# Kernel optimization log

Measured on AMD Instinct MI355X. Metric: run time of the kernel, lower is better.

## Reference

```python
import jax, jax.numpy as jnp
import numpy as np

IMAGE_H, IMAGE_W = 256, 704
Z, Y, X = 128, 8, 128
BOUNDS = (-50.0, 50.0, -5.0, 5.0, -50.0, 50.0)
CENTROID = (0.0, 1.0, 0.0)
EPS_MEAN = 1e-6
EPS_DEPTH = 1e-4


def _compose_rt(R, t):
    M = jnp.zeros(R.shape[:-2] + (4, 4), R.dtype)
    M = M.at[..., :3, :3].set(R)
    M = M.at[..., :3, 3].set(t)
    M = M.at[..., 3, 3].set(1.0)
    return M


def _safe_inverse(M):
    R = M[..., :3, :3]
    t = M[..., :3, 3]
    Rt = jnp.swapaxes(R, -1, -2)
    return _compose_rt(Rt, -jnp.einsum('...ij,...j->...i', Rt, t))


def _apply_4x4(M, xyz):
    # M: (...,4,4), xyz: (...,N,3) -> (...,N,3)
    return jnp.einsum('...ij,...nj->...ni', M[..., :3, :3], xyz) + M[..., None, :3, 3]


def _xyz_camA():
    # Mem2Ref of gridcloud3d: x_ref = x_mem*vox + MIN + vox/2 (bounds shifted by centroid)
    xmin = BOUNDS[0] + CENTROID[0]; xmax = BOUNDS[1] + CENTROID[0]
    ymin = BOUNDS[2] + CENTROID[1]; ymax = BOUNDS[3] + CENTROID[1]
    zmin = BOUNDS[4] + CENTROID[2]; zmax = BOUNDS[5] + CENTROID[2]
    vx = (xmax - xmin) / X; vy = (ymax - ymin) / Y; vz = (zmax - zmin) / Z
    zz, yy, xx = jnp.meshgrid(jnp.arange(Z, dtype=jnp.float32),
                              jnp.arange(Y, dtype=jnp.float32),
                              jnp.arange(X, dtype=jnp.float32), indexing='ij')
    x = xx * vx + xmin + vx / 2.0
    y = yy * vy + ymin + vy / 2.0
    z = zz * vz + zmin + vz / 2.0
    return jnp.stack([x, y, z], -1).reshape(Z * Y * X, 3)  # mem order (Z,Y,X)


def _bilinear_sample(img, px, py):
    # img: (C,H,W); px,py: (N,) pixel coords; zeros padding (grid_sample align_corners=False)
    C, H, W = img.shape
    x0 = jnp.floor(px); y0 = jnp.floor(py)
    dx = px - x0; dy = py - y0
    x0i = x0.astype(jnp.int32); y0i = y0.astype(jnp.int32)
    flat = img.reshape(C, H * W)

    def gather(yi, xi, w):
        inb = (xi >= 0) & (xi < W) & (yi >= 0) & (yi < H)
        idx = jnp.clip(yi, 0, H - 1) * W + jnp.clip(xi, 0, W - 1)
        return flat[:, idx] * (w * inb.astype(img.dtype))

    return (gather(y0i, x0i, (1 - dx) * (1 - dy))
            + gather(y0i, x0i + 1, dx * (1 - dy))
            + gather(y0i + 1, x0i, (1 - dx) * dy)
            + gather(y0i + 1, x0i + 1, dx * dy))  # (C,N)


def _forward(cam_feat, camera2ego, cam_intrinsic, conv_w):
    B, S, C, Hf, Wf = cam_feat.shape
    # velo_T_cams = merge_rt(camera2ego R, t); cam0_T_camXs = inv(velo_T_cams[:,0]) @ velo_T_cams
    velo_T_cams = _compose_rt(camera2ego[..., :3, :3], camera2ego[..., :3, 3])
    cam0_T_velo = _safe_inverse(velo_T_cams[:, 0])
    cam0_T_camXs = jnp.einsum('bij,bsjk->bsik', cam0_T_velo, velo_T_cams)
    camXs_T_cam0 = _safe_inverse(cam0_T_camXs)
    # scale_intrinsics with sy = Hf/H*0.284, sx = Wf/W*0.44
    sy = Hf / float(IMAGE_H) * 0.284
    sx = Wf / float(IMAGE_W) * 0.44
    fx = cam_intrinsic[..., 0, 0] * sx
    fy = cam_intrinsic[..., 1, 1] * sy
    cx = cam_intrinsic[..., 0, 2] * sx
    cy = cam_intrinsic[..., 1, 2] * sy
    K = jnp.zeros((B, S, 4, 4), cam_feat.dtype)
    K = K.at[..., 0, 0].set(fx).at[..., 1, 1].set(fy)
    K = K.at[..., 0, 2].set(cx).at[..., 1, 2].set(cy)
    K = K.at[..., 2, 2].set(1.0).at[..., 3, 3].set(1.0)
    pixB_T_cam0 = jnp.einsum('bsij,bsjk->bsik', K, camXs_T_cam0)

    xyz = _xyz_camA()  # (N,3), N = Z*Y*X
    xyz_camB = _apply_4x4(camXs_T_cam0, xyz[None, None])  # (B,S,N,3)
    z_cam = xyz_camB[..., 2]
    xyz_pix = _apply_4x4(pixB_T_cam0, xyz[None, None])
    depth = jnp.maximum(xyz_pix[..., 2], EPS_DEPTH)
    x_pix = xyz_pix[..., 0] / depth
    y_pix = xyz_pix[..., 1] / depth
    valid = ((x_pix > -0.5) & (x_pix < Wf - 0.5)
             & (y_pix > -0.5) & (y_pix < Hf - 0.5)
             & (z_cam > 0.0)).astype(cam_feat.dtype)
    # normalize_grid2d (clamp [-2,2]) then grid_sample align_corners=False unnormalize
    gx = jnp.clip(2.0 * x_pix / (Wf - 1) - 1.0, -2.0, 2.0)
    gy = jnp.clip(2.0 * y_pix / (Hf - 1) - 1.0, -2.0, 2.0)
    px = ((gx + 1.0) * Wf - 1.0) / 2.0
    py = ((gy + 1.0) * Hf - 1.0) / 2.0

    feats = cam_feat.reshape(B * S, C, Hf, Wf)
    vals = jax.vmap(_bilinear_sample)(feats, px.reshape(B * S, -1), py.reshape(B * S, -1))
    vals = vals.reshape(B, S, C, -1) * valid[:, :, None, :]  # (B,S,C,N)
    mask = (jnp.abs(vals) > 0).astype(vals.dtype)
    feat_mem = jnp.sum(vals * mask, axis=1) / (EPS_MEAN + jnp.sum(mask, axis=1))  # (B,C,N)
    feat_mem = feat_mem.reshape(B, C, Z, Y, X)

    # BEV compress: permute(0,1,3,2,4) -> (B, C*Y, Z, X), conv3x3 (no bias), InstanceNorm2d, GELU
    feat_bev = jnp.transpose(feat_mem, (0, 1, 3, 2, 4)).reshape(B, C * Y, Z, X)
    out = jax.lax.conv_general_dilated(feat_bev, conv_w, (1, 1), ((1, 1), (1, 1)),
                                       dimension_numbers=('NCHW', 'OIHW', 'NCHW'))
    mu = jnp.mean(out, axis=(2, 3), keepdims=True)
    var = jnp.var(out, axis=(2, 3), keepdims=True)
    out = (out - mu) / jnp.sqrt(var + 1e-5)
    return jax.nn.gelu(out, approximate=False)


def setup_inputs() -> dict:
    key = jax.random.key(0)
    k1, k2, k3 = jax.random.split(key, 3)
    B, S, C, Hf, Wf = 1, 6, 128, 32, 88
    cam_feat = jax.random.normal(k1, (B, S, C, Hf, Wf), jnp.float32)
    # rigid camera2ego: yaw rotations about the y axis + small translations
    yaws = jnp.arange(S, dtype=jnp.float32) * (2.0 * jnp.pi / S)
    c, s = jnp.cos(yaws), jnp.sin(yaws)
    zr, on = jnp.zeros_like(c), jnp.ones_like(c)
    R = jnp.stack([jnp.stack([c, zr, s], -1),
                   jnp.stack([zr, on, zr], -1),
                   jnp.stack([-s, zr, c], -1)], -2)  # (S,3,3)
    t = jax.random.normal(k2, (S, 3), jnp.float32) * 0.5
    cam2ego = jnp.zeros((B, S, 4, 4), jnp.float32)
    cam2ego = cam2ego.at[0, :, :3, :3].set(R).at[0, :, :3, 3].set(t).at[0, :, 3, 3].set(1.0)
    K = jnp.zeros((B, S, 4, 4), jnp.float32)
    K = K.at[..., 0, 0].set(600.0).at[..., 1, 1].set(600.0)
    K = K.at[..., 0, 2].set(352.0).at[..., 1, 2].set(128.0)
    K = K.at[..., 2, 2].set(1.0).at[..., 3, 3].set(1.0)
    conv_w = jax.random.normal(k3, (128, 128 * Y, 3, 3), jnp.float32) / np.sqrt(128 * Y * 9.0).astype(np.float32)
    return {"cam_feat": cam_feat, "camera2ego": cam2ego, "cam_intrinsic": K, "conv_w": conv_w}


def reference(cam_feat, camera2ego, cam_intrinsic, conv_w):
    return _forward(cam_feat, camera2ego, cam_intrinsic, conv_w)
```

## Files before the change

kernel.cpp:

```cpp
#include <hip/hip_runtime.h>
#include <hip/hip_bf16.h>
#include <math.h>

#define HF 32
#define WF 88
#define NCAM 6
#define CC 128
#define ZD 128
#define YD 8
#define XD 128

using f32x4  = __attribute__((ext_vector_type(4))) float;
using bf16x8 = __attribute__((ext_vector_type(8))) short;

#define OFF_P    0ull
#define OFF_W    512ull
#define OFF_CAMT (OFF_W + 2359296ull)
#define OFF_F    (OFF_CAMT + 8650752ull)
#define OFF_CONV (OFF_F + 34611200ull)

__global__ __launch_bounds__(64) void k0_mats(const float* __restrict__ cam2ego,
                                              const float* __restrict__ intr,
                                              float* __restrict__ P) {
  int s = threadIdx.x;
  if (s >= NCAM) return;
  const float* M0 = cam2ego;
  const float* Ms = cam2ego + s * 16;
  float Rb[9], tb[3];
  for (int i = 0; i < 3; i++)
    for (int j = 0; j < 3; j++) {
      float v = 0.f;
      for (int k = 0; k < 3; k++) v += Ms[k * 4 + i] * M0[k * 4 + j];
      Rb[i * 3 + j] = v;
    }
  for (int i = 0; i < 3; i++) {
    float v = 0.f;
    for (int k = 0; k < 3; k++) v += Ms[k * 4 + i] * (M0[k * 4 + 3] - Ms[k * 4 + 3]);
    tb[i] = v;
  }
  const float* Ks = intr + s * 16;
  const float sx = (float)WF / 704.0f * 0.44f;
  const float sy = (float)HF / 256.0f * 0.284f;
  const float fx = Ks[0] * sx, fy = Ks[5] * sy;
  const float cx = Ks[2] * sx, cy = Ks[6] * sy;
  float* p = P + s * 12;
  for (int j = 0; j < 3; j++) p[j]     = fx * Rb[j]     + cx * Rb[6 + j];
  p[3]  = fx * tb[0] + cx * tb[2];
  for (int j = 0; j < 3; j++) p[4 + j] = fy * Rb[3 + j] + cy * Rb[6 + j];
  p[7]  = fy * tb[1] + cy * tb[2];
  for (int j = 0; j < 3; j++) p[8 + j] = Rb[6 + j];
  p[11] = tb[2];
}

__global__ __launch_bounds__(128) void k1_transpose(const float* __restrict__ feat,
                                                    __hip_bfloat16* __restrict__ camT) {
  const int b = blockIdx.x;
  const int wq = b & 3;
  const int sh = b >> 2;
  const int c = threadIdx.x;
  const float* src = feat + ((size_t)(sh / HF) * CC + c) * (HF * WF) + (sh % HF) * WF + wq * 22;
  __hip_bfloat16* dst = camT + ((size_t)sh * WF + wq * 22) * CC + c;
  for (int w = 0; w < 22; w++) dst[w * CC] = __float2bfloat16(src[w]);
}

__global__ __launch_bounds__(256) void k1b_packw(const float* __restrict__ w,
                                                 __hip_bfloat16* __restrict__ wp) {
  const int t = blockIdx.x * 256 + threadIdx.x;
  float v[9];
  #pragma unroll
  for (int d = 0; d < 9; d++) v[d] = w[(size_t)t * 9 + d];
  #pragma unroll
  for (int d = 0; d < 9; d++) wp[(size_t)d * 131072 + t] = __float2bfloat16(v[d]);
}

struct Rec { int off[4]; float w[4]; };

__global__ __launch_bounds__(256) void k2_sample(const __hip_bfloat16* __restrict__ camT,
                                                 const float* __restrict__ P,
                                                 __hip_bfloat16* __restrict__ F) {
  const int bz = blockIdx.x / 130;
  const int bx = blockIdx.x % 130;
  const int t = threadIdx.x;
  const int zi = bz - 1, xi = bx - 1;
  const int c = (t & 63) << 1;
  const int yq = t >> 6;
  __hip_bfloat16* Fb = F + (size_t)blockIdx.x * 1024;
  if (zi < 0 || zi >= ZD || xi < 0 || xi >= XD) {
    *reinterpret_cast<unsigned*>(Fb + c * 8 + yq * 2) = 0u;
    *reinterpret_cast<unsigned*>(Fb + (c + 1) * 8 + yq * 2) = 0u;
    return;
  }
  __shared__ Rec recs[48];
  if (t < 48) {
    const int y = t / 6, s = t - y * 6;
    const float* pp = P + s * 12;
    const float vx = 100.0f / 128.0f;
    const float xw = xi * vx - 50.0f + vx * 0.5f;
    const float zw = zi * vx - 50.0f + vx * 0.5f;
    const float yw = y * 1.25f - 4.0f + 0.625f;
    const float zc = pp[8] * xw + pp[9] * yw + pp[10] * zw + pp[11];
    const float xp = pp[0] * xw + pp[1] * yw + pp[2] * zw + pp[3];
    const float yp = pp[4] * xw + pp[5] * yw + pp[6] * zw + pp[7];
    const float dep = fmaxf(zc, 1e-4f);
    const float pxf = xp / dep, pyf = yp / dep;
    const bool valid = (pxf > -0.5f && pxf < (float)WF - 0.5f &&
                        pyf > -0.5f && pyf < (float)HF - 0.5f && zc > 0.0f);
    const float px = pxf * ((float)WF / (float)(WF - 1)) - 0.5f;
    const float py = pyf * ((float)HF / (float)(HF - 1)) - 0.5f;
    const float fx0 = floorf(px), fy0 = floorf(py);
    const float ddx = px - fx0, ddy = py - fy0;
    const int x0i = (int)fx0, y0i = (int)fy0;
    const float vf = valid ? 1.0f : 0.0f;
    float ww[4];
    ww[0] = (1.0f - ddx) * (1.0f - ddy) * vf;
    ww[1] = ddx * (1.0f - ddy) * vf;
    ww[2] = (1.0f - ddx) * ddy * vf;
    ww[3] = ddx * ddy * vf;
    const int cxs[4] = {x0i, x0i + 1, x0i, x0i + 1};
    const int cys[4] = {y0i, y0i, y0i + 1, y0i + 1};
    Rec r;
    #pragma unroll
    for (int k = 0; k < 4; k++) {
      const bool inb = ((unsigned)cxs[k] < WF) && ((unsigned)cys[k] < HF);
      const int xc = min(max(cxs[k], 0), WF - 1);
      const int yc = min(max(cys[k], 0), HF - 1);
      r.w[k] = inb ? ww[k] : 0.0f;
      r.off[k] = (s * (HF * WF) + yc * WF + xc) * CC;
    }
    recs[t] = r;
  }
  __syncthreads();

  float num[2][2] = {{0.f, 0.f}, {0.f, 0.f}};
  int cnt[2] = {0, 0};
  #pragma unroll
  for (int yi = 0; yi < 2; yi++) {
    const int y = yq * 2 + yi;
    for (int s = 0; s < NCAM; s++) {
      const Rec r = recs[y * 6 + s];
      if (r.w[0] == 0.f && r.w[1] == 0.f && r.w[2] == 0.f && r.w[3] == 0.f) continue;
      float v0 = 0.f, v1 = 0.f;
      #pragma unroll
      for (int k = 0; k < 4; k++) {
        const ushort2 uv = *reinterpret_cast<const ushort2*>(&camT[r.off[k] + c]);
        v0 += r.w[k] * __bfloat162float(*reinterpret_cast<const __hip_bfloat16*>(&uv.x));
        v1 += r.w[k] * __bfloat162float(*reinterpret_cast<const __hip_bfloat16*>(&uv.y));
      }
      num[yi][0] += v0;
      num[yi][1] += v1;
      cnt[yi]++;
    }
  }
  #pragma unroll
  for (int j = 0; j < 2; j++) {
    __hip_bfloat16 o[2];
    const float inv0 = 1.0f / (1e-6f + (float)cnt[0]);
    const float inv1 = 1.0f / (1e-6f + (float)cnt[1]);
    o[0] = __float2bfloat16(num[0][j] * inv0);
    o[1] = __float2bfloat16(num[1][j] * inv1);
    *reinterpret_cast<unsigned*>(Fb + (c + j) * 8 + yq * 2) =
        *reinterpret_cast<const unsigned*>(o);
  }
}

__device__ __forceinline__ void load_lds16(const void* g, void* l) {
  __builtin_amdgcn_global_load_lds(
      (const __attribute__((address_space(1))) unsigned int*)g,
      (__attribute__((address_space(3))) unsigned int*)l, 16, 0, 0);
}

#define K3_NT 36

__global__ __launch_bounds__(512) void k3_gemm(const __hip_bfloat16* __restrict__ F,
                                               const __hip_bfloat16* __restrict__ Wp,
                                               float* __restrict__ out0,
                                               float* __restrict__ out1) {
  const int orig = (blockIdx.x & 7) * 32 + (blockIdx.x >> 3);
  const int z = orig & 127;
  const int h = orig >> 7;
  const int ciH = h << 9;
  const int tid = threadIdx.x;
  const int w = tid >> 6;
  const int l = tid & 63;
  const int wm = w >> 2;
  const int wn = w & 3;
  __shared__ __hip_bfloat16 lds[65536];

  f32x4 acc[4][2];
  #pragma unroll
  for (int m = 0; m < 4; m++)
    #pragma unroll
    for (int n = 0; n < 2; n++)
      acc[m][n] = (f32x4){0.f, 0.f, 0.f, 0.f};

  auto stage_sub = [&](int sub) {
    const int base = ((sub >> 1) & 1) * 32768 + (sub & 1) * 16384;
    const int d = sub >> 3;
    const int dz = d / 3, dx = d - dz * 3;
    const int ci0 = ciH + ((sub & 7) << 6);
    const int zbase = (z + dz) * 130 + dx;
    #pragma unroll
    for (int i = 0; i < 2; i++) {
      const int n = w * 128 + i * 64 + l;
      const int row = n >> 3;
      const int q = (n & 7) ^ (row & 7);
      const __hip_bfloat16* src = F + ((size_t)(zbase + row) << 10) + ci0 + (q << 3);
      load_lds16(src, &lds[base + (w * 128 + i * 64) * 8]);
    }
    #pragma unroll
    for (int i = 0; i < 2; i++) {
      const int n = w * 128 + i * 64 + l;
      const int co = n >> 3;
      const int q = (n & 7) ^ (co & 7);
      const __hip_bfloat16* src = Wp + ((size_t)d << 17) + ((size_t)co << 10) + ci0 + (q << 3);
      load_lds16(src, &lds[base + 8192 + (w * 128 + i * 64) * 8]);
    }
  };
  auto stage = [&](int T) { stage_sub(2 * T); stage_sub(2 * T + 1); };

  auto compute_sub = [&](int base) {
    const int r16 = l & 15;
    const int hi = l >> 4;
    #pragma unroll
    for (int kk = 0; kk < 2; kk++) {
      const int c = kk * 4 + hi;
      bf16x8 a[4], b[2];
      #pragma unroll
      for (int m = 0; m < 4; m++) {
        const int r = wm * 64 + m * 16 + r16;
        const int slot = c ^ (r & 7);
        a[m] = *reinterpret_cast<const bf16x8*>(&lds[base + r * 64 + slot * 8]);
      }
      #pragma unroll
      for (int n = 0; n < 2; n++) {
        const int co = wn * 32 + n * 16 + r16;
        const int slot = c ^ (co & 7);
        b[n] = *reinterpret_cast<const bf16x8*>(&lds[base + 8192 + co * 64 + slot * 8]);
      }
      __builtin_amdgcn_s_setprio(1);
      #pragma unroll
      for (int m = 0; m < 4; m++)
        #pragma unroll
        for (int n = 0; n < 2; n++)
          acc[m][n] = __builtin_amdgcn_mfma_f32_16x16x32_bf16(a[m], b[n], acc[m][n], 0, 0, 0);
      __builtin_amdgcn_s_setprio(0);
    }
  };
  auto compute = [&](int T) {
    const int b0 = (T & 1) * 32768;
    compute_sub(b0);
    compute_sub(b0 + 16384);
  };

  stage(0); stage(1);
  asm volatile("s_waitcnt vmcnt(8)" ::: "memory");
  __builtin_amdgcn_s_barrier();

  for (int t = 0; t < K3_NT; ++t) {
    compute(t);
    __builtin_amdgcn_s_barrier();
    if (t + 2 < K3_NT) {
      stage(t + 2);
      asm volatile("s_waitcnt vmcnt(8)" ::: "memory");
    } else {
      asm volatile("s_waitcnt vmcnt(0)" ::: "memory");
    }
    __builtin_amdgcn_s_barrier();
  }

  float* outP = h ? out1 : out0;
  const int r16 = l & 15;
  const int hi = l >> 4;
  #pragma unroll
  for (int m = 0; m < 4; m++) {
    const int xr = wm * 64 + m * 16 + hi * 4;
    #pragma unroll
    for (int n = 0; n < 2; n++) {
      const int co = wn * 32 + n * 16 + r16;
      *reinterpret_cast<f32x4*>(&outP[((size_t)co << 14) + (z << 7) + xr]) = acc[m][n];
    }
  }
}

__device__ __forceinline__ float gelu_exact(float x) {
  return 0.5f * x * (1.0f + erff(x * 0.70710678118654752440f));
}

__global__ __launch_bounds__(256) void k4_ln(const float* __restrict__ c0,
                                             const float* __restrict__ c1,
                                             float* __restrict__ outp) {
  const int co = blockIdx.x;
  const float4* p0 = reinterpret_cast<const float4*>(c0 + ((size_t)co << 14));
  const float4* p1 = reinterpret_cast<const float4*>(c1 + ((size_t)co << 14));
  float4 v[16];
  float s = 0.f, s2 = 0.f;
  #pragma unroll
  for (int i = 0; i < 16; i++) {
    float4 a = p0[threadIdx.x + (i << 8)];
    float4 b = p1[threadIdx.x + (i << 8)];
    float4 t;
    t.x = a.x + b.x; t.y = a.y + b.y; t.z = a.z + b.z; t.w = a.w + b.w;
    v[i] = t;
    s  += t.x + t.y + t.z + t.w;
    s2 += t.x * t.x + t.y * t.y + t.z * t.z + t.w * t.w;
  }
  #pragma unroll
  for (int off = 32; off > 0; off >>= 1) {
    s  += __shfl_down(s, off);
    s2 += __shfl_down(s2, off);
  }
  __shared__ float red[8];
  __shared__ float mb[2];
  const int wv = threadIdx.x >> 6, ln = threadIdx.x & 63;
  if (ln == 0) { red[wv] = s; red[wv + 4] = s2; }
  __syncthreads();
  if (threadIdx.x == 0) {
    float S  = red[0] + red[1] + red[2] + red[3];
    float S2 = red[4] + red[5] + red[6] + red[7];
    float mu = S * (1.0f / 16384.0f);
    float var = S2 * (1.0f / 16384.0f) - mu * mu;
    mb[0] = mu;
    mb[1] = 1.0f / sqrtf(var + 1e-5f);
  }
  __syncthreads();
  const float mu = mb[0], inv = mb[1];
  float4* op = reinterpret_cast<float4*>(outp + ((size_t)co << 14));
  #pragma unroll
  for (int i = 0; i < 16; i++) {
    float4 t = v[i];
    float4 r;
    r.x = gelu_exact((t.x - mu) * inv);
    r.y = gelu_exact((t.y - mu) * inv);
    r.z = gelu_exact((t.z - mu) * inv);
    r.w = gelu_exact((t.w - mu) * inv);
    op[threadIdx.x + (i << 8)] = r;
  }
}

extern "C" void kernel_launch(void* const* d_in, const int* in_sizes, int n_in,
                              void* d_out, int out_size, void* d_ws, size_t ws_size,
                              hipStream_t stream) {
  const float* cam_feat = (const float*)d_in[0];
  const float* cam2ego  = (const float*)d_in[1];
  const float* intr     = (const float*)d_in[2];
  const float* conv_w   = (const float*)d_in[3];
  float* out = (float*)d_out;
  char* ws = (char*)d_ws;

  float*          P     = (float*)(ws + OFF_P);
  __hip_bfloat16* Wp    = (__hip_bfloat16*)(ws + OFF_W);
  __hip_bfloat16* camT  = (__hip_bfloat16*)(ws + OFF_CAMT);
  __hip_bfloat16* F     = (__hip_bfloat16*)(ws + OFF_F);
  float*          conv0 = (float*)(ws + OFF_CONV);
  float*          conv1 = (float*)(ws + OFF_CAMT);

  hipLaunchKernelGGL(k0_mats, dim3(1), dim3(64), 0, stream, cam2ego, intr, P);
  hipLaunchKernelGGL(k1_transpose, dim3(NCAM * HF * 4), dim3(128), 0, stream, cam_feat, camT);
  hipLaunchKernelGGL(k1b_packw, dim3(512), dim3(256), 0, stream, conv_w, Wp);
  hipLaunchKernelGGL(k2_sample, dim3(130 * 130), dim3(256), 0, stream, camT, P, F);
  hipLaunchKernelGGL(k3_gemm, dim3(256), dim3(512), 0, stream, F, Wp, conv0, conv1);
  hipLaunchKernelGGL(k4_ln, dim3(128), dim3(256), 0, stream, conv0, conv1, out);
}
```

Measured before the change: 115.6 us.

## Skip empty voxel columns in sampling and conv GEMM via validity bitmask

The sampling kernel now computes per-(z,x) validity with a ballot, exits early when no camera sees the column, and records validity in a global bitmask. The conv GEMM reads the bitmask for its 3-row z neighbourhood, then skips F loads, LDS reads and MFMAs for 16-wide x groups whose receptive field holds no valid voxels, and skips the whole main loop when nothing is valid. This removes work for geometry that falls outside every camera frustum. The cost is extra atomics, per-wave divergent wait counts and more control flow in the hot loop.

```diff
diff --git a/kernel.cpp b/kernel.cpp
--- a/kernel.cpp
+++ b/kernel.cpp
@@ -18,10 +18,13 @@
 #define OFF_CAMT (OFF_W + 2359296ull)
 #define OFF_F    (OFF_CAMT + 8650752ull)
 #define OFF_CONV (OFF_F + 34611200ull)
+#define OFF_VB   (OFF_CONV + 8388608ull)
 
 __global__ __launch_bounds__(64) void k0_mats(const float* __restrict__ cam2ego,
                                               const float* __restrict__ intr,
-                                              float* __restrict__ P) {
+                                              float* __restrict__ P,
+                                              unsigned* __restrict__ VB) {
+  for (int i = threadIdx.x; i < 512; i += 64) VB[i] = 0u;
   int s = threadIdx.x;
   if (s >= NCAM) return;
   const float* M0 = cam2ego;
@@ -77,7 +80,8 @@
 
 __global__ __launch_bounds__(256) void k2_sample(const __hip_bfloat16* __restrict__ camT,
                                                  const float* __restrict__ P,
-                                                 __hip_bfloat16* __restrict__ F) {
+                                                 __hip_bfloat16* __restrict__ F,
+                                                 unsigned* __restrict__ VB) {
   const int bz = blockIdx.x / 130;
   const int bx = blockIdx.x % 130;
   const int t = threadIdx.x;
@@ -91,6 +95,8 @@
     return;
   }
   __shared__ Rec recs[48];
+  __shared__ int anyv;
+  bool v = false;
   if (t < 48) {
     const int y = t / 6, s = t - y * 6;
     const float* pp = P + s * 12;
@@ -128,8 +134,21 @@
       r.off[k] = (s * (HF * WF) + yc * WF + xc) * CC;
     }
     recs[t] = r;
+    v = (r.w[0] + r.w[1] + r.w[2] + r.w[3]) > 0.0f;
+  }
+  if (t < 64) {
+    unsigned long long m = __ballot(v);
+    if (t == 0) {
+      anyv = (m != 0ull) ? 1 : 0;
+      if (m) atomicOr(&VB[zi * 4 + (xi >> 5)], 1u << (xi & 31));
+    }
   }
   __syncthreads();
+  if (!anyv) {
+    *reinterpret_cast<unsigned*>(Fb + c * 8 + yq * 2) = 0u;
+    *reinterpret_cast<unsigned*>(Fb + (c + 1) * 8 + yq * 2) = 0u;
+    return;
+  }
 
   float num[2][2] = {{0.f, 0.f}, {0.f, 0.f}};
   int cnt[2] = {0, 0};
@@ -173,6 +192,7 @@
 
 __global__ __launch_bounds__(512) void k3_gemm(const __hip_bfloat16* __restrict__ F,
                                                const __hip_bfloat16* __restrict__ Wp,
+                                               const unsigned* __restrict__ VB,
                                                float* __restrict__ out0,
                                                float* __restrict__ out1) {
   const int orig = (blockIdx.x & 7) * 32 + (blockIdx.x >> 3);
@@ -186,6 +206,25 @@
   const int wn = w & 3;
   __shared__ __hip_bfloat16 lds[65536];
 
+  unsigned C[4] = {0u, 0u, 0u, 0u};
+  #pragma unroll
+  for (int dz = -1; dz <= 1; ++dz) {
+    const int zz = z + dz;
+    if (zz < 0 || zz >= ZD) continue;
+    C[0] |= VB[zz * 4 + 0]; C[1] |= VB[zz * 4 + 1];
+    C[2] |= VB[zz * 4 + 2]; C[3] |= VB[zz * 4 + 3];
+  }
+  unsigned gmask = 0;
+  #pragma unroll
+  for (int G = 0; G < 8; ++G) {
+    const int lo = (G * 16 - 1 < 0) ? 0 : G * 16 - 1;
+    const int hi = (G * 16 + 16 > 127) ? 127 : G * 16 + 16;
+    unsigned nz = 0;
+    for (int b = lo; b <= hi; ++b) nz |= (C[b >> 5] >> (b & 31)) & 1u;
+    gmask |= nz << G;
+  }
+  const bool aw = (gmask >> w) & 1;
+
   f32x4 acc[4][2];
   #pragma unroll
   for (int m = 0; m < 4; m++)
@@ -199,13 +238,15 @@
     const int dz = d / 3, dx = d - dz * 3;
     const int ci0 = ciH + ((sub & 7) << 6);
     const int zbase = (z + dz) * 130 + dx;
-    #pragma unroll
-    for (int i = 0; i < 2; i++) {
-      const int n = w * 128 + i * 64 + l;
-      const int row = n >> 3;
-      const int q = (n & 7) ^ (row & 7);
-      const __hip_bfloat16* src = F + ((size_t)(zbase + row) << 10) + ci0 + (q << 3);
-      load_lds16(src, &lds[base + (w * 128 + i * 64) * 8]);
+    if (aw) {
+      #pragma unroll
+      for (int i = 0; i < 2; i++) {
+        const int n = w * 128 + i * 64 + l;
+        const int row = n >> 3;
+        const int q = (n & 7) ^ (row & 7);
+        const __hip_bfloat16* src = F + ((size_t)(zbase + row) << 10) + ci0 + (q << 3);
+        load_lds16(src, &lds[base + (w * 128 + i * 64) * 8]);
+      }
     }
     #pragma unroll
     for (int i = 0; i < 2; i++) {
@@ -227,9 +268,11 @@
       bf16x8 a[4], b[2];
       #pragma unroll
       for (int m = 0; m < 4; m++) {
-        const int r = wm * 64 + m * 16 + r16;
-        const int slot = c ^ (r & 7);
-        a[m] = *reinterpret_cast<const bf16x8*>(&lds[base + r * 64 + slot * 8]);
+        if ((gmask >> (wm * 4 + m)) & 1) {
+          const int r = wm * 64 + m * 16 + r16;
+          const int slot = c ^ (r & 7);
+          a[m] = *reinterpret_cast<const bf16x8*>(&lds[base + r * 64 + slot * 8]);
+        }
       }
       #pragma unroll
       for (int n = 0; n < 2; n++) {
@@ -239,10 +282,13 @@
       }
       __builtin_amdgcn_s_setprio(1);
       #pragma unroll
-      for (int m = 0; m < 4; m++)
-        #pragma unroll
-        for (int n = 0; n < 2; n++)
-          acc[m][n] = __builtin_amdgcn_mfma_f32_16x16x32_bf16(a[m], b[n], acc[m][n], 0, 0, 0);
+      for (int m = 0; m < 4; m++) {
+        if ((gmask >> (wm * 4 + m)) & 1) {
+          #pragma unroll
+          for (int n = 0; n < 2; n++)
+            acc[m][n] = __builtin_amdgcn_mfma_f32_16x16x32_bf16(a[m], b[n], acc[m][n], 0, 0, 0);
+        }
+      }
       __builtin_amdgcn_s_setprio(0);
     }
   };
@@ -252,20 +298,24 @@
     compute_sub(b0 + 16384);
   };
 
-  stage(0); stage(1);
-  asm volatile("s_waitcnt vmcnt(8)" ::: "memory");
-  __builtin_amdgcn_s_barrier();
-
-  for (int t = 0; t < K3_NT; ++t) {
-    compute(t);
+  if (gmask != 0) {
+    stage(0); stage(1);
+    if (aw) asm volatile("s_waitcnt vmcnt(8)" ::: "memory");
+    else    asm volatile("s_waitcnt vmcnt(4)" ::: "memory");
     __builtin_amdgcn_s_barrier();
-    if (t + 2 < K3_NT) {
-      stage(t + 2);
-      asm volatile("s_waitcnt vmcnt(8)" ::: "memory");
-    } else {
-      asm volatile("s_waitcnt vmcnt(0)" ::: "memory");
-    }
-    __builtin_amdgcn_s_barrier();
+
+    for (int t = 0; t < K3_NT; ++t) {
+      compute(t);
+      __builtin_amdgcn_s_barrier();
+      if (t + 2 < K3_NT) {
+        stage(t + 2);
+        if (aw) asm volatile("s_waitcnt vmcnt(8)" ::: "memory");
+        else    asm volatile("s_waitcnt vmcnt(4)" ::: "memory");
+      } else {
+        asm volatile("s_waitcnt vmcnt(0)" ::: "memory");
+      }
+      __builtin_amdgcn_s_barrier();
+    }
   }
 
   float* outP = h ? out1 : out0;
@@ -353,11 +403,12 @@
   __hip_bfloat16* F     = (__hip_bfloat16*)(ws + OFF_F);
   float*          conv0 = (float*)(ws + OFF_CONV);
   float*          conv1 = (float*)(ws + OFF_CAMT);
-
-  hipLaunchKernelGGL(k0_mats, dim3(1), dim3(64), 0, stream, cam2ego, intr, P);
+  unsigned*       VB    = (unsigned*)(ws + OFF_VB);
+
+  hipLaunchKernelGGL(k0_mats, dim3(1), dim3(64), 0, stream, cam2ego, intr, P, VB);
   hipLaunchKernelGGL(k1_transpose, dim3(NCAM * HF * 4), dim3(128), 0, stream, cam_feat, camT);
   hipLaunchKernelGGL(k1b_packw, dim3(512), dim3(256), 0, stream, conv_w, Wp);
-  hipLaunchKernelGGL(k2_sample, dim3(130 * 130), dim3(256), 0, stream, camT, P, F);
-  hipLaunchKernelGGL(k3_gemm, dim3(256), dim3(512), 0, stream, F, Wp, conv0, conv1);
+  hipLaunchKernelGGL(k2_sample, dim3(130 * 130), dim3(256), 0, stream, camT, P, F, VB);
+  hipLaunchKernelGGL(k3_gemm, dim3(256), dim3(512), 0, stream, F, Wp, VB, conv0, conv1);
   hipLaunchKernelGGL(k4_ln, dim3(128), dim3(256), 0, stream, conv0, conv1, out);
 }
```

Result: slower. 147.3 us (+27.4%).
